# Performance work log

Hardware: AMD Instinct MI355X
Metric: run time of the kernel (lower is better)

The kernel has to match this reference:

```python
import jax, jax.numpy as jnp
import numpy as np

B, S1, S2, H = 8, 2048, 2048, 1024

def setup_inputs() -> dict:
    key = jax.random.key(0)
    k1, k2, k3, k4, k5, k6 = jax.random.split(key, 6)
    value = jax.random.normal(k1, (B, S1, H), dtype=jnp.float32)
    key_t = jax.random.normal(k2, (B, S2, H), dtype=jnp.float32)
    query = jax.random.normal(k3, (B, S1, H), dtype=jnp.float32)
    mask = jax.random.randint(k4, (B, S1, S2), 0, 2).astype(jnp.bool_)
    # Linear(hidden, hidden) params, torch default init scale
    bound = 1.0 / np.sqrt(H)
    W = jax.random.uniform(k5, (H, H), minval=-bound, maxval=bound, dtype=jnp.float32)
    b = jax.random.uniform(k6, (H,), minval=-bound, maxval=bound, dtype=jnp.float32)
    return {"value": value, "key": key_t, "query": query, "mask": mask, "W": W, "b": b}

def reference(value, key, query, mask, W, b):
    # q_proj = query @ W^T + b  (torch Linear)
    q_proj = jnp.einsum('bqh,oh->bqo', query, W) + b            # [B,S1,H]
    attn = jnp.einsum('bqh,bkh->bqk', q_proj, key)               # [B,S1,S2]
    attn = jnp.where(mask, -jnp.inf, attn)
    attn = jnp.transpose(attn, (0, 2, 1))                        # [B,S2,S1]
    weights = jax.nn.softmax(attn, axis=-1)                      # softmax over S1
    context = jnp.einsum('bks,bsh->bkh', weights, value)         # [B,S2,H]
    return context, weights
```

## Files before the change

### kernel.cpp

```cpp
#include <hip/hip_runtime.h>

#define B_  8
#define S1_ 2048
#define S2_ 2048
#define H_  1024

typedef unsigned short u16;
typedef __attribute__((ext_vector_type(8))) short short8;
typedef __attribute__((ext_vector_type(4))) float f32x4;

__device__ __forceinline__ float b2f(u16 u) {
  union { unsigned int i; float f; } v; v.i = ((unsigned int)u) << 16; return v.f;
}
__device__ __forceinline__ u16 f2b(float f) {
  union { float f; unsigned int i; } v; v.f = f;
  unsigned int r = v.i + 0x7fffu + ((v.i >> 16) & 1u);
  return (u16)(r >> 16);
}

__device__ __forceinline__ int swz(int row, int kk) {
  return (row * 32 + kk) ^ (((row >> 1) & 3) << 3);
}

__device__ __forceinline__ void cvt8_split(float4 va, float4 vb, short8* hi, short8* lo) {
  float x[8] = {va.x, va.y, va.z, va.w, vb.x, vb.y, vb.z, vb.w};
  short8 h, l;
#pragma unroll
  for (int e = 0; e < 8; ++e) {
    u16 hb = f2b(x[e]);
    h[e] = (short)hb;
    l[e] = (short)f2b(x[e] - b2f(hb));
  }
  *hi = h; *lo = l;
}
__device__ __forceinline__ short8 cvt8(float4 va, float4 vb) {
  float x[8] = {va.x, va.y, va.z, va.w, vb.x, vb.y, vb.z, vb.w};
  short8 h;
#pragma unroll
  for (int e = 0; e < 8; ++e) h[e] = (short)f2b(x[e]);
  return h;
}

__device__ __forceinline__ void g2l16(const void* g, void* lds) {
  __builtin_amdgcn_global_load_lds(
      (const __attribute__((address_space(1))) unsigned int*)g,
      (__attribute__((address_space(3))) unsigned int*)lds, 16, 0, 0);
}

template<bool ADD_BIAS, bool DO_MASK, bool SPLIT, bool OUTSPLIT>
__global__ __launch_bounds__(256)
void gemm_bf(const u16* __restrict__ Ahi, const u16* __restrict__ Alo, long sA, int lda,
             const u16* __restrict__ Bhi, const u16* __restrict__ Blo, long sB, int ldb,
             const float* __restrict__ bias,
             const int* __restrict__ mask, long sMask, int mask_ld,
             float* __restrict__ Cf, u16* __restrict__ Chi, u16* __restrict__ Clo,
             long sC, int ldc, int K)
{
  constexpr int NP = SPLIT ? 4 : 2;
  __shared__ __align__(16) union {
    u16 tile[2][NP][128 * 32];
    unsigned char m[128][128];
  } sh;

  const int t    = threadIdx.x;
  const int lane = t & 63;
  const int wv   = t >> 6;
  const int wm   = wv >> 1, wn = wv & 1;

  const int nbx = gridDim.x, nby = gridDim.y;
  const int id  = blockIdx.x + nbx * (blockIdx.y + nby * blockIdx.z);
  const int cpx = (nbx * nby * (int)gridDim.z) >> 3;
  const int sid = (id & 7) * cpx + (id >> 3);
  const int bx  = sid % nbx;
  const int rem = sid / nbx;
  const int by  = rem % nby;
  const int batch = rem / nby;
  const int m0 = bx * 128;
  const int n0 = by * 128;

  const u16* Ah = Ahi + (long)batch * sA + (long)m0 * lda;
  const u16* Bh = Bhi + (long)batch * sB + (long)n0 * ldb;
  const u16* Al = SPLIT ? (Alo + (long)batch * sA + (long)m0 * lda) : nullptr;
  const u16* Bl = SPLIT ? (Blo + (long)batch * sB + (long)n0 * ldb) : nullptr;

  f32x4 acc[4][4];
#pragma unroll
  for (int i = 0; i < 4; ++i)
#pragma unroll
    for (int j = 0; j < 4; ++j)
      acc[i][j] = (f32x4){0.f, 0.f, 0.f, 0.f};

  const int fr = lane & 15;
  const int kg = lane >> 4;

  int srow[2], soff[2], sdst[2];
#pragma unroll
  for (int half = 0; half < 2; ++half) {
    int c = half * 256 + wv * 64 + lane;
    int row = c >> 2;
    srow[half] = row;
    soff[half] = (((c & 3) ^ ((row >> 1) & 3)) * 8);
    sdst[half] = (half * 256 + wv * 64) * 8;
  }

  auto STAGE = [&](int kc, int bufi) {
#pragma unroll
    for (int half = 0; half < 2; ++half) {
      const int ga = srow[half] * lda + kc + soff[half];
      const int gb = srow[half] * ldb + kc + soff[half];
      g2l16(Ah + ga, &sh.tile[bufi][0][sdst[half]]);
      g2l16(Bh + gb, &sh.tile[bufi][1][sdst[half]]);
      if (SPLIT) {
        g2l16(Al + ga, &sh.tile[bufi][2][sdst[half]]);
        g2l16(Bl + gb, &sh.tile[bufi][3][sdst[half]]);
      }
    }
  };

  STAGE(0, 0);
  __syncthreads();
  int cur = 0;

  for (int kc = 0; kc < K; kc += 32) {
    if (kc + 32 < K) STAGE(kc + 32, cur ^ 1);

    short8 afh[4], bfh[4];
#pragma unroll
    for (int i = 0; i < 4; ++i)
      afh[i] = *(const short8*)&sh.tile[cur][0][swz(wm * 64 + i * 16 + fr, kg * 8)];
#pragma unroll
    for (int j = 0; j < 4; ++j)
      bfh[j] = *(const short8*)&sh.tile[cur][1][swz(wn * 64 + j * 16 + fr, kg * 8)];

    if (SPLIT) {
      short8 afl[4], bfl[4];
#pragma unroll
      for (int i = 0; i < 4; ++i)
        afl[i] = *(const short8*)&sh.tile[cur][2][swz(wm * 64 + i * 16 + fr, kg * 8)];
#pragma unroll
      for (int j = 0; j < 4; ++j)
        bfl[j] = *(const short8*)&sh.tile[cur][3][swz(wn * 64 + j * 16 + fr, kg * 8)];
      __builtin_amdgcn_s_setprio(1);
#pragma unroll
      for (int i = 0; i < 4; ++i)
#pragma unroll
        for (int j = 0; j < 4; ++j) {
          acc[i][j] = __builtin_amdgcn_mfma_f32_16x16x32_bf16(afh[i], bfh[j], acc[i][j], 0, 0, 0);
          acc[i][j] = __builtin_amdgcn_mfma_f32_16x16x32_bf16(afh[i], bfl[j], acc[i][j], 0, 0, 0);
          acc[i][j] = __builtin_amdgcn_mfma_f32_16x16x32_bf16(afl[i], bfh[j], acc[i][j], 0, 0, 0);
        }
      __builtin_amdgcn_s_setprio(0);
    } else {
      __builtin_amdgcn_s_setprio(1);
#pragma unroll
      for (int i = 0; i < 4; ++i)
#pragma unroll
        for (int j = 0; j < 4; ++j)
          acc[i][j] = __builtin_amdgcn_mfma_f32_16x16x32_bf16(afh[i], bfh[j], acc[i][j], 0, 0, 0);
      __builtin_amdgcn_s_setprio(0);
    }

    __syncthreads();
    cur ^= 1;
  }

  if (DO_MASK) {
    const int* mb = mask + (long)batch * sMask;
#pragma unroll
    for (int it = 0; it < 16; ++it) {
      int ql = it * 8 + (t >> 5);
      int kl = (t & 31) * 4;
      int4 mv = *(const int4*)(mb + (long)(n0 + ql) * mask_ld + (m0 + kl));
      sh.m[kl + 0][ql] = (unsigned char)(mv.x != 0);
      sh.m[kl + 1][ql] = (unsigned char)(mv.y != 0);
      sh.m[kl + 2][ql] = (unsigned char)(mv.z != 0);
      sh.m[kl + 3][ql] = (unsigned char)(mv.w != 0);
    }
    __syncthreads();
  }

  float bv[4];
  if (ADD_BIAS) {
#pragma unroll
    for (int j = 0; j < 4; ++j)
      bv[j] = bias[n0 + wn * 64 + j * 16 + fr];
  }

#pragma unroll
  for (int i = 0; i < 4; ++i) {
#pragma unroll
    for (int r = 0; r < 4; ++r) {
      int row = wm * 64 + i * 16 + (lane >> 4) * 4 + r;
      long gro = (long)batch * sC + (long)(m0 + row) * ldc + n0;
#pragma unroll
      for (int j = 0; j < 4; ++j) {
        int col = wn * 64 + j * 16 + fr;
        float v = acc[i][j][r];
        if (ADD_BIAS) v += bv[j];
        if (OUTSPLIT) {
          u16 hb = f2b(v);
          Chi[gro + col] = hb;
          Clo[gro + col] = f2b(v - b2f(hb));
        } else {
          if (DO_MASK && sh.m[row][col]) v = -1e30f;
          Cf[gro + col] = v;
        }
      }
    }
  }
}

template<bool ADD_BIAS, bool DO_MASK, bool SPLIT, bool BTR>
__global__ __launch_bounds__(256)
void gemm_k(const float* __restrict__ A, long sA,
            const float* __restrict__ B, long sB, int ldb,
            const float* __restrict__ bias,
            const int* __restrict__ mask, long sMask, int mask_ld,
            float* __restrict__ C, long sC, int ldc, int K)
{
  __shared__ __align__(16) union {
    u16 tile[SPLIT ? 4 : 2][128 * 32];
    unsigned char m[128][128];
  } sh;

  const int t    = threadIdx.x;
  const int lane = t & 63;
  const int wv   = t >> 6;
  const int wm   = wv >> 1, wn = wv & 1;
  const int batch = blockIdx.z;
  const int m0 = blockIdx.x * 128;
  const int n0 = blockIdx.y * 128;

  const float* Ab = A + (long)batch * sA + (long)m0 * K;
  const float* Bb = B + (long)batch * sB + (BTR ? (long)n0 : (long)n0 * ldb);

  f32x4 acc[4][4];
#pragma unroll
  for (int i = 0; i < 4; ++i)
#pragma unroll
    for (int j = 0; j < 4; ++j)
      acc[i][j] = (f32x4){0.f, 0.f, 0.f, 0.f};

  const int c0 = t,       r0 = c0 >> 2, o0 = (c0 & 3) * 8;
  const int c1 = t + 256, r1 = c1 >> 2, o1 = (c1 & 3) * 8;

  const int fr = lane & 15;
  const int kg = lane >> 4;

  for (int kc = 0; kc < K; kc += 32) {
    float4 a00 = *(const float4*)(Ab + (long)r0 * K + kc + o0);
    float4 a01 = *(const float4*)(Ab + (long)r0 * K + kc + o0 + 4);
    float4 a10 = *(const float4*)(Ab + (long)r1 * K + kc + o1);
    float4 a11 = *(const float4*)(Ab + (long)r1 * K + kc + o1 + 4);
    float4 bb[4];
    float btv[2][8];
    if (BTR) {
#pragma unroll
      for (int p = 0; p < 2; ++p)
#pragma unroll
        for (int e = 0; e < 8; ++e)
          btv[p][e] = Bb[(long)(kc + wv * 8 + e) * ldb + lane + p * 64];
    } else {
      bb[0] = *(const float4*)(Bb + (long)r0 * ldb + kc + o0);
      bb[1] = *(const float4*)(Bb + (long)r0 * ldb + kc + o0 + 4);
      bb[2] = *(const float4*)(Bb + (long)r1 * ldb + kc + o1);
      bb[3] = *(const float4*)(Bb + (long)r1 * ldb + kc + o1 + 4);
    }
    __syncthreads();

    if (SPLIT) {
      short8 h, l;
      cvt8_split(a00, a01, &h, &l);
      *(short8*)&sh.tile[0][swz(r0, o0)] = h;  *(short8*)&sh.tile[2][swz(r0, o0)] = l;
      cvt8_split(a10, a11, &h, &l);
      *(short8*)&sh.tile[0][swz(r1, o1)] = h;  *(short8*)&sh.tile[2][swz(r1, o1)] = l;
      cvt8_split(bb[0], bb[1], &h, &l);
      *(short8*)&sh.tile[1][swz(r0, o0)] = h;  *(short8*)&sh.tile[3][swz(r0, o0)] = l;
      cvt8_split(bb[2], bb[3], &h, &l);
      *(short8*)&sh.tile[1][swz(r1, o1)] = h;  *(short8*)&sh.tile[3][swz(r1, o1)] = l;
    } else {
      *(short8*)&sh.tile[0][swz(r0, o0)] = cvt8(a00, a01);
      *(short8*)&sh.tile[0][swz(r1, o1)] = cvt8(a10, a11);
      if (BTR) {
#pragma unroll
        for (int p = 0; p < 2; ++p) {
          short8 h;
#pragma unroll
          for (int e = 0; e < 8; ++e) h[e] = (short)f2b(btv[p][e]);
          *(short8*)&sh.tile[1][swz(lane + p * 64, wv * 8)] = h;
        }
      } else {
        *(short8*)&sh.tile[1][swz(r0, o0)] = cvt8(bb[0], bb[1]);
        *(short8*)&sh.tile[1][swz(r1, o1)] = cvt8(bb[2], bb[3]);
      }
    }
    __syncthreads();

    short8 afh[4], bfh[4];
#pragma unroll
    for (int i = 0; i < 4; ++i)
      afh[i] = *(const short8*)&sh.tile[0][swz(wm * 64 + i * 16 + fr, kg * 8)];
#pragma unroll
    for (int j = 0; j < 4; ++j)
      bfh[j] = *(const short8*)&sh.tile[1][swz(wn * 64 + j * 16 + fr, kg * 8)];

    if (SPLIT) {
      short8 afl[4], bfl[4];
#pragma unroll
      for (int i = 0; i < 4; ++i)
        afl[i] = *(const short8*)&sh.tile[2][swz(wm * 64 + i * 16 + fr, kg * 8)];
#pragma unroll
      for (int j = 0; j < 4; ++j)
        bfl[j] = *(const short8*)&sh.tile[3][swz(wn * 64 + j * 16 + fr, kg * 8)];
#pragma unroll
      for (int i = 0; i < 4; ++i)
#pragma unroll
        for (int j = 0; j < 4; ++j) {
          acc[i][j] = __builtin_amdgcn_mfma_f32_16x16x32_bf16(afh[i], bfh[j], acc[i][j], 0, 0, 0);
          acc[i][j] = __builtin_amdgcn_mfma_f32_16x16x32_bf16(afh[i], bfl[j], acc[i][j], 0, 0, 0);
          acc[i][j] = __builtin_amdgcn_mfma_f32_16x16x32_bf16(afl[i], bfh[j], acc[i][j], 0, 0, 0);
        }
    } else {
#pragma unroll
      for (int i = 0; i < 4; ++i)
#pragma unroll
        for (int j = 0; j < 4; ++j)
          acc[i][j] = __builtin_amdgcn_mfma_f32_16x16x32_bf16(afh[i], bfh[j], acc[i][j], 0, 0, 0);
    }
  }

  if (DO_MASK) {
    __syncthreads();
    const int* mb = mask + (long)batch * sMask;
#pragma unroll
    for (int it = 0; it < 16; ++it) {
      int ql = it * 8 + (t >> 5);
      int kl = (t & 31) * 4;
      int4 mv = *(const int4*)(mb + (long)(n0 + ql) * mask_ld + (m0 + kl));
      sh.m[kl + 0][ql] = (unsigned char)(mv.x != 0);
      sh.m[kl + 1][ql] = (unsigned char)(mv.y != 0);
      sh.m[kl + 2][ql] = (unsigned char)(mv.z != 0);
      sh.m[kl + 3][ql] = (unsigned char)(mv.w != 0);
    }
    __syncthreads();
  }

  float bv[4];
  if (ADD_BIAS) {
#pragma unroll
    for (int j = 0; j < 4; ++j)
      bv[j] = bias[n0 + wn * 64 + j * 16 + fr];
  }

#pragma unroll
  for (int i = 0; i < 4; ++i) {
#pragma unroll
    for (int r = 0; r < 4; ++r) {
      int row = wm * 64 + i * 16 + (lane >> 4) * 4 + r;
      long gro = (long)batch * sC + (long)(m0 + row) * ldc + n0;
#pragma unroll
      for (int j = 0; j < 4; ++j) {
        int col = wn * 64 + j * 16 + fr;
        float v = acc[i][j][r];
        if (ADD_BIAS) v += bv[j];
        if (DO_MASK && sh.m[row][col]) v = -1e30f;
        C[gro + col] = v;
      }
    }
  }
}

__global__ __launch_bounds__(256)
void conv_split(const float* __restrict__ in, u16* __restrict__ hi, u16* __restrict__ lo)
{
  long i = ((long)blockIdx.x * 256 + threadIdx.x) * 8;
  float4 v0 = *(const float4*)(in + i);
  float4 v1 = *(const float4*)(in + i + 4);
  short8 h, l;
  cvt8_split(v0, v1, &h, &l);
  *(short8*)(hi + i) = h;
  *(short8*)(lo + i) = l;
}

__global__ __launch_bounds__(256)
void transpose_conv(const float* __restrict__ v, u16* __restrict__ vt)
{
  __shared__ u16 tl[64][66];
  const int b  = blockIdx.z;
  const int s0 = blockIdx.x * 64, h0 = blockIdx.y * 64;
  const int tr = threadIdx.x >> 4;
  const int tc = (threadIdx.x & 15) * 4;
  const float* vb = v + ((long)b * S1_ + s0) * H_ + h0;
#pragma unroll
  for (int q = 0; q < 4; ++q) {
    int r = tr + q * 16;
    float4 x = *(const float4*)(vb + (long)r * H_ + tc);
    tl[r][tc + 0] = f2b(x.x); tl[r][tc + 1] = f2b(x.y);
    tl[r][tc + 2] = f2b(x.z); tl[r][tc + 3] = f2b(x.w);
  }
  __syncthreads();
  u16* ob = vt + ((long)b * H_ + h0) * S1_ + s0;
#pragma unroll
  for (int q = 0; q < 4; ++q) {
    int hr = tr + q * 16;
    unsigned int w0 = (unsigned int)tl[tc + 0][hr] | ((unsigned int)tl[tc + 1][hr] << 16);
    unsigned int w1 = (unsigned int)tl[tc + 2][hr] | ((unsigned int)tl[tc + 3][hr] << 16);
    uint2 w = {w0, w1};
    *(uint2*)(ob + (long)hr * S1_ + tc) = w;
  }
}

__global__ __launch_bounds__(256)
void softmax_rows(float* __restrict__ scores, u16* __restrict__ wbf)
{
  const long row = blockIdx.x;
  float* p = scores + row * (long)S1_;
  const int t = threadIdx.x;
  const int lane = t & 63, wv = t >> 6;

  float4 v0 = *(const float4*)(p + t * 8);
  float4 v1 = *(const float4*)(p + t * 8 + 4);
  float x[8] = {v0.x, v0.y, v0.z, v0.w, v1.x, v1.y, v1.z, v1.w};

  float m = x[0];
#pragma unroll
  for (int q = 1; q < 8; ++q) m = fmaxf(m, x[q]);
#pragma unroll
  for (int o = 32; o; o >>= 1) m = fmaxf(m, __shfl_xor(m, o));
  __shared__ float rb[4], sb[4];
  if (lane == 0) rb[wv] = m;
  __syncthreads();
  m = fmaxf(fmaxf(rb[0], rb[1]), fmaxf(rb[2], rb[3]));

  float e[8]; float s = 0.f;
#pragma unroll
  for (int q = 0; q < 8; ++q) { e[q] = __expf(x[q] - m); s += e[q]; }
#pragma unroll
  for (int o = 32; o; o >>= 1) s += __shfl_xor(s, o);
  if (lane == 0) sb[wv] = s;
  __syncthreads();
  s = sb[0] + sb[1] + sb[2] + sb[3];
  float inv = 1.f / s;

  float w[8];
#pragma unroll
  for (int q = 0; q < 8; ++q) w[q] = e[q] * inv;
  float4 o0 = {w[0], w[1], w[2], w[3]};
  float4 o1 = {w[4], w[5], w[6], w[7]};
  *(float4*)(p + t * 8)     = o0;
  *(float4*)(p + t * 8 + 4) = o1;

  if (wbf != nullptr) {
    short8 hb;
#pragma unroll
    for (int q = 0; q < 8; ++q) hb[q] = (short)f2b(w[q]);
    *(short8*)(wbf + row * (long)S1_ + t * 8) = hb;
  }
}

extern "C" void kernel_launch(void* const* d_in, const int* in_sizes, int n_in,
                              void* d_out, int out_size, void* d_ws, size_t ws_size,
                              hipStream_t stream)
{
  const float* value = (const float*)d_in[0];
  const float* key   = (const float*)d_in[1];
  const float* query = (const float*)d_in[2];
  const int*   mask  = (const int*)d_in[3];
  const float* W     = (const float*)d_in[4];
  const float* bias  = (const float*)d_in[5];

  float* ctx = (float*)d_out;
  float* wts = ctx + (size_t)B_ * S2_ * H_;

  dim3 blk(256);
  const size_t MB = 1024ull * 1024ull;

  if (ws_size >= 132 * MB && d_ws != nullptr) {
    u16* pjhi = (u16*)ctx;
    u16* pjlo = (u16*)ctx + (size_t)B_ * S1_ * H_;

    char* ws = (char*)d_ws;
    u16* khi = (u16*)(ws);
    u16* klo = (u16*)(ws + 32 * MB);
    u16* wbf = (u16*)(ws);
    u16* qhi = (u16*)(ws + 64 * MB);
    u16* qlo = (u16*)(ws + 96 * MB);
    u16* vT  = (u16*)(ws + 64 * MB);
    u16* whi = (u16*)(ws + 128 * MB);
    u16* wlo = (u16*)(ws + 130 * MB);

    conv_split<<<dim3((B_ * S1_ * H_) / 2048), blk, 0, stream>>>(query, qhi, qlo);
    conv_split<<<dim3((B_ * S2_ * H_) / 2048), blk, 0, stream>>>(key, khi, klo);
    conv_split<<<dim3((H_ * H_) / 2048), blk, 0, stream>>>(W, whi, wlo);

    gemm_bf<true, false, true, true><<<dim3((B_ * S1_) / 128, H_ / 128, 1), blk, 0, stream>>>(
        qhi, qlo, 0, H_, whi, wlo, 0, H_, bias,
        nullptr, 0, 0, nullptr, pjhi, pjlo, 0, H_, H_);

    transpose_conv<<<dim3(S1_ / 64, H_ / 64, B_), blk, 0, stream>>>(value, vT);

    gemm_bf<false, true, true, false><<<dim3(S2_ / 128, S1_ / 128, B_), blk, 0, stream>>>(
        khi, klo, (long)S2_ * H_, H_, pjhi, pjlo, (long)S1_ * H_, H_, nullptr,
        mask, (long)S1_ * S2_, S2_, wts, nullptr, nullptr, (long)S2_ * S1_, S1_, H_);

    softmax_rows<<<dim3(B_ * S2_), blk, 0, stream>>>(wts, wbf);

    gemm_bf<false, false, false, false><<<dim3(S2_ / 128, H_ / 128, B_), blk, 0, stream>>>(
        wbf, nullptr, (long)S2_ * S1_, S1_, vT, nullptr, (long)H_ * S1_, S1_, nullptr,
        nullptr, 0, 0, ctx, nullptr, nullptr, (long)S2_ * H_, H_, S1_);
  } else {
    float* qproj = ctx;

    gemm_k<true, false, true, false><<<dim3((B_ * S1_) / 128, H_ / 128, 1), blk, 0, stream>>>(
        query, 0, W, 0, H_, bias, nullptr, 0, 0, qproj, 0, H_, H_);

    gemm_k<false, true, true, false><<<dim3(S2_ / 128, S1_ / 128, B_), blk, 0, stream>>>(
        key, (long)S2_ * H_, qproj, (long)S1_ * H_, H_, nullptr,
        mask, (long)S1_ * S2_, S2_, wts, (long)S2_ * S1_, S1_, H_);

    softmax_rows<<<dim3(B_ * S2_), blk, 0, stream>>>(wts, nullptr);

    gemm_k<false, false, false, true><<<dim3(S2_ / 128, H_ / 128, B_), blk, 0, stream>>>(
        wts, (long)S2_ * S1_, value, (long)S1_ * H_, H_, nullptr,
        nullptr, 0, 0, ctx, (long)S2_ * H_, H_, S1_);
  }
}
```

Measured before the change: 878.1 us.

## Pack attention mask into bitmask and fuse conversion kernels into one launch

Adds a pre-pass that packs the int32 mask into 64-bit ballot bitmasks, so the masked score GEMM reads one u64 per column per wave instead of staging int tiles through LDS with a barrier. The three hi/lo split conversion kernels are merged into one launch to cut launch overhead. The bitmask path is only taken if the workspace is at least 136 MB. Otherwise it falls back to the old LDS mask path.

```diff
diff --git a/kernel.cpp b/kernel.cpp
--- a/kernel.cpp
+++ b/kernel.cpp
@@ -6,6 +6,7 @@
 #define H_  1024
 
 typedef unsigned short u16;
+typedef unsigned long long u64;
 typedef __attribute__((ext_vector_type(8))) short short8;
 typedef __attribute__((ext_vector_type(4))) float f32x4;
 
@@ -47,12 +48,12 @@
       (__attribute__((address_space(3))) unsigned int*)lds, 16, 0, 0);
 }
 
-template<bool ADD_BIAS, bool DO_MASK, bool SPLIT, bool OUTSPLIT>
+template<bool ADD_BIAS, int MASKMODE, bool SPLIT, bool OUTSPLIT>
 __global__ __launch_bounds__(256)
 void gemm_bf(const u16* __restrict__ Ahi, const u16* __restrict__ Alo, long sA, int lda,
              const u16* __restrict__ Bhi, const u16* __restrict__ Blo, long sB, int ldb,
              const float* __restrict__ bias,
-             const int* __restrict__ mask, long sMask, int mask_ld,
+             const void* __restrict__ maskp, long sMask, int mask_ld,
              float* __restrict__ Cf, u16* __restrict__ Chi, u16* __restrict__ Clo,
              long sC, int ldc, int K)
 {
@@ -164,8 +165,8 @@
     cur ^= 1;
   }
 
-  if (DO_MASK) {
-    const int* mb = mask + (long)batch * sMask;
+  if (MASKMODE == 1) {
+    const int* mb = (const int*)maskp + (long)batch * sMask;
 #pragma unroll
     for (int it = 0; it < 16; ++it) {
       int ql = it * 8 + (t >> 5);
@@ -179,6 +180,16 @@
     __syncthreads();
   }
 
+  u64 mbits[4];
+  if (MASKMODE == 2) {
+    const u64* mb = (const u64*)maskp + (long)batch * sMask;
+#pragma unroll
+    for (int j = 0; j < 4; ++j) {
+      int col = wn * 64 + j * 16 + fr;
+      mbits[j] = mb[(long)(n0 + col) * mask_ld + (m0 >> 6) + wm];
+    }
+  }
+
   float bv[4];
   if (ADD_BIAS) {
 #pragma unroll
@@ -190,7 +201,8 @@
   for (int i = 0; i < 4; ++i) {
 #pragma unroll
     for (int r = 0; r < 4; ++r) {
-      int row = wm * 64 + i * 16 + (lane >> 4) * 4 + r;
+      int rloc = i * 16 + kg * 4 + r;
+      int row  = wm * 64 + rloc;
       long gro = (long)batch * sC + (long)(m0 + row) * ldc + n0;
 #pragma unroll
       for (int j = 0; j < 4; ++j) {
@@ -202,7 +214,8 @@
           Chi[gro + col] = hb;
           Clo[gro + col] = f2b(v - b2f(hb));
         } else {
-          if (DO_MASK && sh.m[row][col]) v = -1e30f;
+          if (MASKMODE == 1 && sh.m[row][col]) v = -1e30f;
+          if (MASKMODE == 2 && ((mbits[j] >> rloc) & 1ull)) v = -1e30f;
           Cf[gro + col] = v;
         }
       }
@@ -371,9 +384,34 @@
 }
 
 __global__ __launch_bounds__(256)
-void conv_split(const float* __restrict__ in, u16* __restrict__ hi, u16* __restrict__ lo)
-{
-  long i = ((long)blockIdx.x * 256 + threadIdx.x) * 8;
+void pack_mask(const int* __restrict__ mask, u64* __restrict__ pm)
+{
+  const long row = blockIdx.x;
+  const int wv = threadIdx.x >> 6, lane = threadIdx.x & 63;
+  const int* mr = mask + row * (long)S2_;
+  u64* pr = pm + row * (long)(S2_ / 64);
+#pragma unroll
+  for (int i = 0; i < 8; ++i) {
+    int base = (wv * 8 + i) * 64;
+    int x = mr[base + lane];
+    u64 bal = __ballot(x != 0);
+    if (lane == 0) pr[wv * 8 + i] = bal;
+  }
+}
+
+__global__ __launch_bounds__(256)
+void conv_split3(const float* __restrict__ q, u16* __restrict__ qhi, u16* __restrict__ qlo,
+                 const float* __restrict__ k, u16* __restrict__ khi, u16* __restrict__ klo,
+                 const float* __restrict__ w, u16* __restrict__ whi, u16* __restrict__ wlo)
+{
+  const int NQ = (B_ * S1_ * H_) / 2048;
+  const int NK = (B_ * S2_ * H_) / 2048;
+  int bb = blockIdx.x;
+  const float* in; u16 *hi, *lo; long i;
+  if (bb < NQ)           { in = q; hi = qhi; lo = qlo; i = (long)bb; }
+  else if (bb < NQ + NK) { in = k; hi = khi; lo = klo; i = (long)(bb - NQ); }
+  else                   { in = w; hi = whi; lo = wlo; i = (long)(bb - NQ - NK); }
+  i = (i * 256 + threadIdx.x) * 8;
   float4 v0 = *(const float4*)(in + i);
   float4 v1 = *(const float4*)(in + i + 4);
   short8 h, l;
@@ -476,6 +514,8 @@
   const size_t MB = 1024ull * 1024ull;
 
   if (ws_size >= 132 * MB && d_ws != nullptr) {
+    const bool BITMASK = (ws_size >= 136 * MB);
+
     u16* pjhi = (u16*)ctx;
     u16* pjlo = (u16*)ctx + (size_t)B_ * S1_ * H_;
 
@@ -488,24 +528,34 @@
     u16* vT  = (u16*)(ws + 64 * MB);
     u16* whi = (u16*)(ws + 128 * MB);
     u16* wlo = (u16*)(ws + 130 * MB);
-
-    conv_split<<<dim3((B_ * S1_ * H_) / 2048), blk, 0, stream>>>(query, qhi, qlo);
-    conv_split<<<dim3((B_ * S2_ * H_) / 2048), blk, 0, stream>>>(key, khi, klo);
-    conv_split<<<dim3((H_ * H_) / 2048), blk, 0, stream>>>(W, whi, wlo);
-
-    gemm_bf<true, false, true, true><<<dim3((B_ * S1_) / 128, H_ / 128, 1), blk, 0, stream>>>(
+    u64* pm  = (u64*)(ws + 132 * MB);
+
+    conv_split3<<<dim3((B_ * S1_ * H_) / 2048 + (B_ * S2_ * H_) / 2048 + (H_ * H_) / 2048),
+                  blk, 0, stream>>>(query, qhi, qlo, key, khi, klo, W, whi, wlo);
+    if (BITMASK)
+      pack_mask<<<dim3(B_ * S1_), blk, 0, stream>>>(mask, pm);
+
+    gemm_bf<true, 0, true, true><<<dim3((B_ * S1_) / 128, H_ / 128, 1), blk, 0, stream>>>(
         qhi, qlo, 0, H_, whi, wlo, 0, H_, bias,
         nullptr, 0, 0, nullptr, pjhi, pjlo, 0, H_, H_);
 
     transpose_conv<<<dim3(S1_ / 64, H_ / 64, B_), blk, 0, stream>>>(value, vT);
 
-    gemm_bf<false, true, true, false><<<dim3(S2_ / 128, S1_ / 128, B_), blk, 0, stream>>>(
-        khi, klo, (long)S2_ * H_, H_, pjhi, pjlo, (long)S1_ * H_, H_, nullptr,
-        mask, (long)S1_ * S2_, S2_, wts, nullptr, nullptr, (long)S2_ * S1_, S1_, H_);
+    if (BITMASK) {
+      gemm_bf<false, 2, true, false><<<dim3(S2_ / 128, S1_ / 128, B_), blk, 0, stream>>>(
+          khi, klo, (long)S2_ * H_, H_, pjhi, pjlo, (long)S1_ * H_, H_, nullptr,
+          pm, (long)S1_ * (S2_ / 64), S2_ / 64,
+          wts, nullptr, nullptr, (long)S2_ * S1_, S1_, H_);
+    } else {
+      gemm_bf<false, 1, true, false><<<dim3(S2_ / 128, S1_ / 128, B_), blk, 0, stream>>>(
+          khi, klo, (long)S2_ * H_, H_, pjhi, pjlo, (long)S1_ * H_, H_, nullptr,
+          mask, (long)S1_ * S2_, S2_,
+          wts, nullptr, nullptr, (long)S2_ * S1_, S1_, H_);
+    }
 
     softmax_rows<<<dim3(B_ * S2_), blk, 0, stream>>>(wts, wbf);
 
-    gemm_bf<false, false, false, false><<<dim3(S2_ / 128, H_ / 128, B_), blk, 0, stream>>>(
+    gemm_bf<false, 0, false, false><<<dim3(S2_ / 128, H_ / 128, B_), blk, 0, stream>>>(
         wbf, nullptr, (long)S2_ * S1_, S1_, vT, nullptr, (long)H_ * S1_, S1_, nullptr,
         nullptr, 0, 0, ctx, nullptr, nullptr, (long)S2_ * H_, H_, S1_);
   } else {
```

New measurement: 887.2 us. No clear change (+1.0%).
